# Kernel optimization log

Measured on AMD Instinct MI355X. Metric: run time of the kernel, lower is better.

## Reference

```python
import jax, jax.numpy as jnp
import numpy as np

B, K, D, N_SENSES = 512, 32, 768, 200000
NEG_INF = -1e30


def setup_inputs() -> dict:
    key = jax.random.key(0)
    k1, k2, k3 = jax.random.split(key, 3)
    reps = jax.random.normal(k1, (B, D), dtype=jnp.float32)
    weight = jax.random.normal(k2, (N_SENSES, D), dtype=jnp.float32) * 0.02
    bias = jax.random.normal(k3, (N_SENSES,), dtype=jnp.float32) * 0.02
    # Ragged candidate sets: each sample has a variable number of candidate
    # senses in [2, K], remainder padded with -1 (as in the torch code).
    rng = np.random.default_rng(0)
    lengths = rng.integers(2, K + 1, size=B)
    ids = rng.integers(0, N_SENSES, size=(B, K)).astype(np.int64)
    pos = np.arange(K)[None, :]
    ids = np.where(pos < lengths[:, None], ids, -1)
    targets = (rng.integers(0, 1 << 30, size=B) % lengths).astype(np.int64)
    return {
        "reps": reps,
        "weight": weight,
        "bias": bias,
        "sense_ids": jnp.asarray(ids),
        "target_ids": jnp.asarray(targets),
    }


def reference(reps, weight, bias, sense_ids, target_ids):
    # mask of valid (non -1) candidates, [B, K]
    mask = sense_ids >= 0
    ids = jnp.where(mask, sense_ids, 0)
    # ragged gather of candidate rows: [B, K, D] and [B, K]
    w = weight[ids]
    b = bias[ids]
    # per-sample small matvec + bias -> logits [B, K]
    logits = jnp.einsum("bkd,bd->bk", w, reps) + b
    logits = jnp.where(mask, logits, NEG_INF)
    # cross-entropy per sample, summed then divided by B (== mean)
    logp = jax.nn.log_softmax(logits, axis=-1)
    nll = -jnp.take_along_axis(logp, target_ids[:, None], axis=-1)[:, 0]
    loss = jnp.mean(nll)
    correct = jnp.argmax(logits, axis=-1) == target_ids
    return loss, correct
```

## Files before the change

kernel.cpp:

```cpp
#include <hip/hip_runtime.h>
#include <math.h>

#define BB 512
#define KK 32
#define DD 768
#define NEG_INF (-1e30f)

__global__ __launch_bounds__(256) void cbert_logits_kernel(
    const float* __restrict__ reps,
    const float* __restrict__ weight,
    const float* __restrict__ bias,
    const int*   __restrict__ sense_ids,
    const int*   __restrict__ target_ids,
    float* __restrict__ out,
    float* __restrict__ nll_ws)
{
    __shared__ float4 s_repv[DD / 4];
    __shared__ float  s_logits[KK];

    const int b   = blockIdx.x;
    const int tid = threadIdx.x;

    const float4* repv = reinterpret_cast<const float4*>(reps + (size_t)b * DD);
    for (int i = tid; i < DD / 4; i += 256) s_repv[i] = repv[i];
    __syncthreads();

    const int wave = tid >> 6;
    const int lane = tid & 63;

    for (int k = wave; k < KK; k += 4) {
        const int id = sense_ids[b * KK + k];
        float logit;
        if (id < 0) {
            logit = NEG_INF;
        } else {
            const float4* wrow =
                reinterpret_cast<const float4*>(weight + (size_t)id * DD);
            float acc = 0.0f;
            #pragma unroll
            for (int j = 0; j < 3; ++j) {
                const float4 w4 = wrow[j * 64 + lane];
                const float4 r4 = s_repv[j * 64 + lane];
                acc += w4.x * r4.x + w4.y * r4.y + w4.z * r4.z + w4.w * r4.w;
            }
            #pragma unroll
            for (int off = 32; off >= 1; off >>= 1)
                acc += __shfl_down(acc, off, 64);
            logit = acc + bias[id];
        }
        if (lane == 0) s_logits[k] = logit;
    }
    __syncthreads();

    if (tid == 0) {
        float m = s_logits[0];
        int   am = 0;
        for (int k = 1; k < KK; ++k) {
            const float v = s_logits[k];
            if (v > m) { m = v; am = k; }
        }
        float se = 0.0f;
        for (int k = 0; k < KK; ++k) se += expf(s_logits[k] - m);
        const int tgt = target_ids[b];
        const float nll = -(s_logits[tgt] - m - logf(se));
        nll_ws[b]    = nll;
        out[1 + b]   = (am == tgt) ? 1.0f : 0.0f;
    }
}

__global__ __launch_bounds__(64) void cbert_loss_kernel(
    const float* __restrict__ nll_ws, float* __restrict__ out)
{
    const int lane = threadIdx.x;
    float acc = 0.0f;
    for (int i = lane; i < BB; i += 64) acc += nll_ws[i];
    #pragma unroll
    for (int off = 32; off >= 1; off >>= 1)
        acc += __shfl_down(acc, off, 64);
    if (lane == 0) out[0] = acc / (float)BB;
}

extern "C" void kernel_launch(void* const* d_in, const int* in_sizes, int n_in,
                              void* d_out, int out_size, void* d_ws, size_t ws_size,
                              hipStream_t stream) {
    const float* reps       = (const float*)d_in[0];
    const float* weight     = (const float*)d_in[1];
    const float* bias       = (const float*)d_in[2];
    const int*   sense_ids  = (const int*)d_in[3];
    const int*   target_ids = (const int*)d_in[4];
    float* out    = (float*)d_out;
    float* nll_ws = (float*)d_ws;

    cbert_logits_kernel<<<BB, 256, 0, stream>>>(
        reps, weight, bias, sense_ids, target_ids, out, nll_ws);
    cbert_loss_kernel<<<1, 64, 0, stream>>>(nll_ws, out);
}
```

Measured before the change: 667.2 us.

## Spread candidate dot products across blocks and move softmax into a wave-parallel kernel

The logits kernel now launches one wave per candidate (4096 blocks of 4 waves) instead of one block per sample, and reads reps straight from global memory instead of staging it in shared memory, so more blocks are in flight to hide the random-row gather latency. The single-thread serial softmax/argmax is replaced by a second kernel where each wave reduces one sample's 32 logits with shuffles, and the loss mean is built with atomicAdd, which removes the separate loss kernel. In exchange, logits go through a workspace round-trip, reps is re-read once per candidate, and the atomic float summation makes the loss order nondeterministic.

```diff
diff --git a/kernel.cpp b/kernel.cpp
--- a/kernel.cpp
+++ b/kernel.cpp
@@ -5,79 +5,82 @@
 #define KK 32
 #define DD 768
 #define NEG_INF (-1e30f)
+#define NCAND (BB * KK)
 
 __global__ __launch_bounds__(256) void cbert_logits_kernel(
     const float* __restrict__ reps,
     const float* __restrict__ weight,
     const float* __restrict__ bias,
     const int*   __restrict__ sense_ids,
-    const int*   __restrict__ target_ids,
-    float* __restrict__ out,
-    float* __restrict__ nll_ws)
+    float* __restrict__ logits_ws,
+    float* __restrict__ out)
 {
-    __shared__ float4 s_repv[DD / 4];
-    __shared__ float  s_logits[KK];
+    if (blockIdx.x == 0 && threadIdx.x == 0) out[0] = 0.0f;
 
-    const int b   = blockIdx.x;
-    const int tid = threadIdx.x;
+    const int c    = blockIdx.x * 4 + (threadIdx.x >> 6);
+    const int lane = threadIdx.x & 63;
+    const int b    = c >> 5;
 
-    const float4* repv = reinterpret_cast<const float4*>(reps + (size_t)b * DD);
-    for (int i = tid; i < DD / 4; i += 256) s_repv[i] = repv[i];
-    __syncthreads();
-
-    const int wave = tid >> 6;
-    const int lane = tid & 63;
-
-    for (int k = wave; k < KK; k += 4) {
-        const int id = sense_ids[b * KK + k];
-        float logit;
-        if (id < 0) {
-            logit = NEG_INF;
-        } else {
-            const float4* wrow =
-                reinterpret_cast<const float4*>(weight + (size_t)id * DD);
-            float acc = 0.0f;
-            #pragma unroll
-            for (int j = 0; j < 3; ++j) {
-                const float4 w4 = wrow[j * 64 + lane];
-                const float4 r4 = s_repv[j * 64 + lane];
-                acc += w4.x * r4.x + w4.y * r4.y + w4.z * r4.z + w4.w * r4.w;
-            }
-            #pragma unroll
-            for (int off = 32; off >= 1; off >>= 1)
-                acc += __shfl_down(acc, off, 64);
-            logit = acc + bias[id];
+    const int id = sense_ids[c];
+    float logit = NEG_INF;
+    if (id >= 0) {
+        const float4* wrow = reinterpret_cast<const float4*>(weight + (size_t)id * DD);
+        const float4* rrow = reinterpret_cast<const float4*>(reps   + (size_t)b  * DD);
+        float acc = 0.0f;
+        #pragma unroll
+        for (int j = 0; j < 3; ++j) {
+            const float4 w4 = wrow[j * 64 + lane];
+            const float4 r4 = rrow[j * 64 + lane];
+            acc += w4.x * r4.x + w4.y * r4.y + w4.z * r4.z + w4.w * r4.w;
         }
-        if (lane == 0) s_logits[k] = logit;
+        #pragma unroll
+        for (int off = 32; off >= 1; off >>= 1)
+            acc += __shfl_xor(acc, off, 64);
+        logit = acc + bias[id];
     }
-    __syncthreads();
-
-    if (tid == 0) {
-        float m = s_logits[0];
-        int   am = 0;
-        for (int k = 1; k < KK; ++k) {
-            const float v = s_logits[k];
-            if (v > m) { m = v; am = k; }
-        }
-        float se = 0.0f;
-        for (int k = 0; k < KK; ++k) se += expf(s_logits[k] - m);
-        const int tgt = target_ids[b];
-        const float nll = -(s_logits[tgt] - m - logf(se));
-        nll_ws[b]    = nll;
-        out[1 + b]   = (am == tgt) ? 1.0f : 0.0f;
-    }
+    if (lane == 0) logits_ws[c] = logit;
 }
 
-__global__ __launch_bounds__(64) void cbert_loss_kernel(
-    const float* __restrict__ nll_ws, float* __restrict__ out)
+__global__ __launch_bounds__(512) void cbert_ce_kernel(
+    const float* __restrict__ logits_ws,
+    const int*   __restrict__ target_ids,
+    float* __restrict__ out)
 {
-    const int lane = threadIdx.x;
-    float acc = 0.0f;
-    for (int i = lane; i < BB; i += 64) acc += nll_ws[i];
+    const int wave = threadIdx.x >> 6;
+    const int lane = threadIdx.x & 63;
+    const int b    = blockIdx.x * 8 + wave;
+
+    float myv;
+    int   myi;
+    if (lane < KK) {
+        myv = logits_ws[b * KK + lane];
+        myi = lane;
+    } else {
+        myv = -INFINITY;
+        myi = 64;
+    }
+
+    float mv = myv;
+    int   mi = myi;
     #pragma unroll
-    for (int off = 32; off >= 1; off >>= 1)
-        acc += __shfl_down(acc, off, 64);
-    if (lane == 0) out[0] = acc / (float)BB;
+    for (int off = 1; off < 64; off <<= 1) {
+        const float ov = __shfl_xor(mv, off, 64);
+        const int   oi = __shfl_xor(mi, off, 64);
+        if (ov > mv || (ov == mv && oi < mi)) { mv = ov; mi = oi; }
+    }
+
+    float e = expf(myv - mv);
+    #pragma unroll
+    for (int off = 1; off < 64; off <<= 1)
+        e += __shfl_xor(e, off, 64);
+
+    if (lane == 0) {
+        const int   tgt = target_ids[b];
+        const float lt  = logits_ws[b * KK + tgt];
+        const float nll = -(lt - mv - logf(e));
+        atomicAdd(&out[0], nll * (1.0f / (float)BB));
+        out[1 + b] = (mi == tgt) ? 1.0f : 0.0f;
+    }
 }
 
 extern "C" void kernel_launch(void* const* d_in, const int* in_sizes, int n_in,
@@ -88,10 +91,10 @@
     const float* bias       = (const float*)d_in[2];
     const int*   sense_ids  = (const int*)d_in[3];
     const int*   target_ids = (const int*)d_in[4];
-    float* out    = (float*)d_out;
-    float* nll_ws = (float*)d_ws;
+    float* out       = (float*)d_out;
+    float* logits_ws = (float*)d_ws;
 
-    cbert_logits_kernel<<<BB, 256, 0, stream>>>(
-        reps, weight, bias, sense_ids, target_ids, out, nll_ws);
-    cbert_loss_kernel<<<1, 64, 0, stream>>>(nll_ws, out);
+    cbert_logits_kernel<<<NCAND / 4, 256, 0, stream>>>(
+        reps, weight, bias, sense_ids, logits_ws, out);
+    cbert_ce_kernel<<<BB / 8, 512, 0, stream>>>(logits_ws, target_ids, out);
 }
```

Measured after the change: 667.4 us. No clear change (+0.0%).
